# Performance work log

Hardware: AMD Instinct MI355X
Metric: run time of the kernel (lower is better)

The kernel has to match this reference:

```python
import jax, jax.numpy as jnp
import numpy as np

CONV = 49
LAYERS = 4
EDGE_DIM = 10
MSG_H = 3
EPS = 1e-5

def setup_inputs() -> dict:
    key = jax.random.key(0)
    ks = jax.random.split(key, 16)
    N, E = 25000, 50000
    x = jax.random.normal(ks[0], (N, 56), dtype=jnp.float32)
    edge_index = jax.random.randint(ks[1], (2, E), 0, N, dtype=jnp.int64)
    edge_attr = jax.random.uniform(ks[2], (E, EDGE_DIM), dtype=jnp.float32)
    s = 0.1
    return {
        'x': x,
        'edge_index': edge_index,
        'edge_attr': edge_attr,
        'lin_w': jax.random.normal(ks[3], (56, CONV), dtype=jnp.float32) * s,
        'lin_b': jnp.zeros((CONV,), jnp.float32),
        'mlp_w1': jax.random.normal(ks[4], (LAYERS, EDGE_DIM, MSG_H), dtype=jnp.float32) * s,
        'mlp_b1': jnp.zeros((LAYERS, MSG_H), jnp.float32),
        'mlp_w2': jax.random.normal(ks[5], (LAYERS, MSG_H, CONV * CONV), dtype=jnp.float32) * s,
        'mlp_b2': jnp.zeros((LAYERS, CONV * CONV), jnp.float32),
        'root_w': jax.random.normal(ks[6], (LAYERS, CONV, CONV), dtype=jnp.float32) * s,
        'conv_b': jnp.zeros((LAYERS, CONV), jnp.float32),
        'bn_gamma': jnp.ones((LAYERS, CONV), jnp.float32),
        'bn_beta': jnp.zeros((LAYERS, CONV), jnp.float32),
    }

def reference(x, edge_index, edge_attr, lin_w, lin_b, mlp_w1, mlp_b1, mlp_w2, mlp_b2, root_w, conv_b, bn_gamma, bn_beta):
    N = x.shape[0]
    E = edge_attr.shape[0]
    src, dst = edge_index[0], edge_index[1]
    # input atom projection
    h = jax.nn.leaky_relu(x @ lin_w + lin_b)
    # scatter-mean denominator (count clamped at 1, as in PyG)
    deg = jax.ops.segment_sum(jnp.ones((E,), h.dtype), dst, num_segments=N)
    denom = jnp.maximum(deg, 1.0)[:, None]
    xs = [h]
    for l in range(LAYERS):
        hc = xs[l]
        # edge MLP -> per-edge [CONV, CONV] weight matrix
        ew = jax.nn.relu(edge_attr @ mlp_w1[l] + mlp_b1[l]) @ mlp_w2[l] + mlp_b2[l]
        ew = ew.reshape(E, CONV, CONV)
        # gather src features, per-edge matvec, scatter-mean to dst
        msg = jnp.einsum('ei,eio->eo', hc[src], ew)
        agg = jax.ops.segment_sum(msg, dst, num_segments=N) / denom
        # NNConv root weight + bias
        out = agg + hc @ root_w[l] + conv_b[l]
        # BatchNorm1d (training-mode batch statistics, biased variance)
        mu = out.mean(axis=0)
        var = out.var(axis=0)
        out = (out - mu) * jax.lax.rsqrt(var + EPS) * bn_gamma[l] + bn_beta[l]
        out = jax.nn.leaky_relu(out)
        xs.append(out)
    # JK = 'sum' over layers 0..num_layer-1 (first 4 entries of x_list)
    return xs[0] + xs[1] + xs[2] + xs[3]
```

## Files before the change

kernel.cpp:

```cpp
#include <hip/hip_runtime.h>


#define N 25000
#define E 50000
#define C 49
#define C2 196
#define SLOPE 0.01f
#define BPN 32
#define GK 2
#define NPB 8
#define NREP 8

__device__ __forceinline__ float leaky(float v) { return v > 0.f ? v : SLOPE * v; }
#define RFL(x) __builtin_amdgcn_readfirstlane(x)

__global__ void deg_kernel(const int* __restrict__ ei, int* __restrict__ deg) {
    int e = blockIdx.x * 256 + threadIdx.x;
    if (e < E) atomicAdd(&deg[ei[E + e]], 1);
}

__global__ __launch_bounds__(1024) void scan_kernel(const int* __restrict__ deg,
                                                    int* __restrict__ rowptr) {
    __shared__ int wsum[16];
    int t = threadIdx.x, lane = t & 63, wv = t >> 6;
    int base = t * 25;
    int loc[25];
    int run = 0;
#pragma unroll
    for (int i = 0; i < 25; i++) {
        loc[i] = run;
        int idx = base + i;
        run += (idx < N) ? deg[idx] : 0;
    }
    int inc = run;
#pragma unroll
    for (int s = 1; s < 64; s <<= 1) {
        int v = __shfl_up(inc, s, 64);
        if (lane >= s) inc += v;
    }
    if (lane == 63) wsum[wv] = inc;
    __syncthreads();
    if (t < 16) {
        int v = wsum[t];
#pragma unroll
        for (int s = 1; s < 16; s <<= 1) {
            int u = __shfl_up(v, s, 64);
            if (t >= s) v += u;
        }
        wsum[t] = v;
    }
    __syncthreads();
    int pbase = inc - run + (wv ? wsum[wv - 1] : 0);
#pragma unroll
    for (int i = 0; i < 25; i++) {
        int idx = base + i;
        if (idx <= N) rowptr[idx] = pbase + loc[i];
    }
}

__global__ void scatter_kernel(const int* __restrict__ ei, const float* __restrict__ ea,
                               const float* __restrict__ w1, const float* __restrict__ b1,
                               const int* __restrict__ rowptr, int* __restrict__ cnt,
                               float* __restrict__ PK) {
    int e = blockIdx.x * 256 + threadIdx.x;
    if (e >= E) return;
    int s = ei[e], d = ei[E + e];
    int pos = rowptr[d] + atomicAdd(&cnt[d], 1);
    float a[10];
#pragma unroll
    for (int j = 0; j < 10; j++) a[j] = ea[e * 10 + j];
#pragma unroll
    for (int l = 0; l < 3; l++) {
        float tk[3];
#pragma unroll
        for (int k = 0; k < 3; k++) {
            float acc = b1[l * 3 + k];
#pragma unroll
            for (int j = 0; j < 10; j++) acc += a[j] * w1[l * 30 + j * 3 + k];
            tk[k] = fmaxf(acc, 0.f);
        }
        float4 rec = make_float4(__int_as_float(s), tk[0], tk[1], tk[2]);
        *reinterpret_cast<float4*>(PK + ((size_t)l * E + pos) * 4) = rec;
    }
}

__device__ __forceinline__ void gemm_phase(const float (*hs)[52], int base, int nv,
                                           const float* __restrict__ w2,
                                           const float* __restrict__ b2,
                                           const float* __restrict__ rw,
                                           const float* __restrict__ cb,
                                           float* __restrict__ U, float* __restrict__ Rt,
                                           int t) {
    if (t >= 245) return;
    int k = t / C, o = t % C;
    const float* Wp = (k < 3 ? w2 + k * (C * C) : (k == 3 ? b2 : rw)) + o;
    float bias = (k == 4) ? cb[o] : 0.f;
    float w[52];
#pragma unroll
    for (int i = 0; i < C; i++) w[i] = Wp[i * C];
    w[49] = w[50] = w[51] = 0.f;
#pragma unroll 2
    for (int n = 0; n < nv; n++) {
        float acc = bias;
#pragma unroll
        for (int i4 = 0; i4 < 13; i4++) {
            float4 hv = *reinterpret_cast<const float4*>(&hs[n][i4 * 4]);
            acc += hv.x * w[i4 * 4] + hv.y * w[i4 * 4 + 1] + hv.z * w[i4 * 4 + 2] +
                   hv.w * w[i4 * 4 + 3];
        }
        if (k < 4) U[(size_t)(base + n) * C2 + o * 4 + k] = acc;
        else Rt[(size_t)(base + n) * C + o] = acc;
    }
}

__global__ __launch_bounds__(256) void h2u0_kernel(
    const float* __restrict__ x, const float* __restrict__ lw, const float* __restrict__ lb,
    const float* __restrict__ w2, const float* __restrict__ b2, const float* __restrict__ rw,
    const float* __restrict__ cb, float* __restrict__ out, float* __restrict__ U,
    float* __restrict__ Rt) {
    __shared__ float xs[BPN][56];
    __shared__ float hs[BPN][52];
    int t = threadIdx.x, base = blockIdx.x * BPN;
    int nv = min(BPN, N - base);
    for (int e = t; e < nv * 56; e += 256) xs[e / 56][e % 56] = x[(size_t)base * 56 + e];
    for (int j = t; j < BPN * 3; j += 256) hs[j / 3][C + (j % 3)] = 0.f;
    __syncthreads();
    int r = t >> 6, c = t & 63;
    if (c < C) {
        float w[56];
#pragma unroll
        for (int i = 0; i < 56; i++) w[i] = lw[i * C + c];
        float bias = lb[c];
        for (int n = r; n < nv; n += 4) {
            float acc = bias;
#pragma unroll
            for (int i4 = 0; i4 < 14; i4++) {
                float4 hv = *reinterpret_cast<const float4*>(&xs[n][i4 * 4]);
                acc += hv.x * w[i4 * 4] + hv.y * w[i4 * 4 + 1] + hv.z * w[i4 * 4 + 2] +
                       hv.w * w[i4 * 4 + 3];
            }
            acc = leaky(acc);
            out[(size_t)(base + n) * C + c] = acc;
            hs[n][c] = acc;
        }
    }
    __syncthreads();
    gemm_phase(hs, base, nv, w2, b2, rw, cb, U, Rt, t);
}

__global__ __launch_bounds__(256) void uni_kernel(
    const float* __restrict__ in, const float* __restrict__ stRaw,
    const float* __restrict__ gm, const float* __restrict__ bt,
    const float* __restrict__ w2, const float* __restrict__ b2,
    const float* __restrict__ rw, const float* __restrict__ cb,
    float* __restrict__ out, float* __restrict__ U, float* __restrict__ Rt) {
    __shared__ float hs[BPN][52];
    __shared__ float scl[64], sft[64];
    int t = threadIdx.x, base = blockIdx.x * BPN;
    int nv = min(BPN, N - base);
    if (t < C) {
        float S = 0.f, Q = 0.f;
#pragma unroll
        for (int r = 0; r < NREP; r++) {
            S += stRaw[r * 128 + t];
            Q += stRaw[r * 128 + 64 + t];
        }
        float mu = S * (1.0f / N);
        float var = Q * (1.0f / N) - mu * mu;
        float sc = rsqrtf(var + 1e-5f) * gm[t];
        scl[t] = sc;
        sft[t] = bt[t] - mu * sc;
    }
    for (int j = t; j < BPN * 3; j += 256) hs[j / 3][C + j % 3] = 0.f;
    __syncthreads();
    for (int e = t; e < nv * C; e += 256) {
        int n = e / C, i = e % C;
        float v = in[(size_t)base * C + e];
        v = leaky(v * scl[i] + sft[i]);
        out[(size_t)base * C + e] += v;
        hs[n][i] = v;
    }
    __syncthreads();
    gemm_phase(hs, base, nv, w2, b2, rw, cb, U, Rt, t);
}

__global__ __launch_bounds__(256) void gathpre_kernel(
    const int* __restrict__ rowptr, const float* __restrict__ PK, const float* __restrict__ U,
    const float* __restrict__ Rt, float* __restrict__ pre, float* __restrict__ st) {
    __shared__ float red[8][64];
    int t = threadIdx.x, wv = t >> 6, c = t & 63;
    int n0 = blockIdx.x * NPB + wv * GK;
    float s = 0.f, q = 0.f;
    int nend = min(n0 + GK, N);
    const float4* PK4 = reinterpret_cast<const float4*>(PK);
    for (int n = n0; n < nend; n++) {
        int nu = RFL(n);
        int j0 = RFL(rowptr[nu]);
        int j1 = RFL(rowptr[nu + 1]);
        if (c < C) {
            float rr = Rt[(size_t)nu * C + c];
            float a0 = 0.f, a1 = 0.f, a2 = 0.f, a3 = 0.f;
            int jc = max(j1 - 1, j0);
            int j = j0;
            do {
#define EDGE_TERM(K, AK)                                                          \
                {                                                                 \
                    int jj = min(j + K, jc);                                      \
                    float4 m = PK4[jj];                                           \
                    int sidx = RFL(__float_as_int(m.x));                          \
                    sidx = min(max(sidx, 0), N - 1);                              \
                    float4 u = *reinterpret_cast<const float4*>(                  \
                        U + (size_t)sidx * C2 + c * 4);                           \
                    float sc = (j + K < j1) ? 1.f : 0.f;                          \
                    AK += sc * (m.y * u.x + m.z * u.y + m.w * u.z + u.w);         \
                }
                EDGE_TERM(0, a0)
                EDGE_TERM(1, a1)
                EDGE_TERM(2, a2)
                EDGE_TERM(3, a3)
#undef EDGE_TERM
                j += 4;
            } while (j < j1);
            float inv = 1.0f / fmaxf((float)(j1 - j0), 1.0f);
            float acc = (a0 + a1 + a2 + a3) * inv + rr;
            pre[(size_t)nu * C + c] = acc;
            s += acc;
            q += acc * acc;
        }
    }
    red[wv][c] = s;
    red[4 + wv][c] = q;
    __syncthreads();
    if (t < C) {
        float* slot = st + (blockIdx.x & (NREP - 1)) * 128;
        float S = red[0][t] + red[1][t] + red[2][t] + red[3][t];
        float Q = red[4][t] + red[5][t] + red[6][t] + red[7][t];
        atomicAdd(&slot[t], S);
        atomicAdd(&slot[64 + t], Q);
    }
}

__global__ __launch_bounds__(256) void fnorm_kernel(const float* __restrict__ pre,
                                                    const float* __restrict__ stRaw,
                                                    const float* __restrict__ gm,
                                                    const float* __restrict__ bt,
                                                    float* __restrict__ out) {
    __shared__ float scl[64], sft[64];
    int t = threadIdx.x;
    if (t < C) {
        float S = 0.f, Q = 0.f;
#pragma unroll
        for (int r = 0; r < NREP; r++) {
            S += stRaw[r * 128 + t];
            Q += stRaw[r * 128 + 64 + t];
        }
        float mu = S * (1.0f / N);
        float var = Q * (1.0f / N) - mu * mu;
        float sc = rsqrtf(var + 1e-5f) * gm[t];
        scl[t] = sc;
        sft[t] = bt[t] - mu * sc;
    }
    __syncthreads();
    for (int idx = blockIdx.x * 256 + t; idx < N * C; idx += gridDim.x * 256) {
        int c = idx % C;
        out[idx] += leaky(pre[idx] * scl[c] + sft[c]);
    }
}

extern "C" void kernel_launch(void* const* d_in, const int* in_sizes, int n_in,
                              void* d_out, int out_size, void* d_ws, size_t ws_size,
                              hipStream_t stream) {
    const float* x  = (const float*)d_in[0];
    const int* ei   = (const int*)d_in[1];
    const float* ea = (const float*)d_in[2];
    const float* lw = (const float*)d_in[3];
    const float* lb = (const float*)d_in[4];
    const float* w1 = (const float*)d_in[5];
    const float* b1 = (const float*)d_in[6];
    const float* w2 = (const float*)d_in[7];
    const float* b2 = (const float*)d_in[8];
    const float* rw = (const float*)d_in[9];
    const float* cb = (const float*)d_in[10];
    const float* gm = (const float*)d_in[11];
    const float* bt = (const float*)d_in[12];
    float* out = (float*)d_out;

    float* ws     = (float*)d_ws;
    int*   deg    = (int*)ws;
    int*   cnt    = deg + N;
    float* st     = (float*)(cnt + N);
    int*   rowptr = (int*)(st + 3 * 1024);
    float* PK     = (float*)(rowptr + N + 1);
    float* agg    = PK + (size_t)12 * E;
    float* Rt     = agg + (size_t)N * C;
    float* U      = Rt + (size_t)N * C;

    hipMemsetAsync(deg, 0, (size_t)(2 * N + 3 * 1024) * sizeof(int), stream);
    deg_kernel<<<(E + 255) / 256, 256, 0, stream>>>(ei, deg);
    scan_kernel<<<1, 1024, 0, stream>>>(deg, rowptr);
    scatter_kernel<<<(E + 255) / 256, 256, 0, stream>>>(ei, ea, w1, b1, rowptr, cnt, PK);
    h2u0_kernel<<<(N + BPN - 1) / BPN, 256, 0, stream>>>(x, lw, lb, w2, b2, rw, cb, out, U, Rt);

    const int GPB = (N + NPB - 1) / NPB;
    for (int l = 0; l < 3; l++) {
        if (l > 0) {
            uni_kernel<<<(N + BPN - 1) / BPN, 256, 0, stream>>>(
                agg, st + (size_t)(l - 1) * 1024, gm + (l - 1) * C, bt + (l - 1) * C,
                w2 + (size_t)l * 3 * C * C, b2 + (size_t)l * C * C,
                rw + (size_t)l * C * C, cb + l * C, out, U, Rt);
        }
        gathpre_kernel<<<GPB, 256, 0, stream>>>(
            rowptr, PK + (size_t)l * E * 4, U, Rt, agg, st + (size_t)l * 1024);
    }
    fnorm_kernel<<<512, 256, 0, stream>>>(agg, st + 2 * 1024, gm + 2 * C, bt + 2 * C, out);
}
```

Measured before the change: 240.2 us.

## Fuse degree count, scan and memset into one kernel; merge scatter with input projection

Replaces the memset, degree-atomic kernel and scan kernel with a single one-block kernel that counts degrees in shared memory in two halves, scans them, and initializes rowptr, cnt and the stats buffer. The edge scatter kernel and the input projection kernel are merged into one launch split by block index, with cnt pre-seeded to rowptr so the scatter needs only one atomic. This cuts launches and small serial kernels, but the single-block degree pass reads all edges twice from one CU, which may be slower than the parallel atomic version.

```diff
diff --git a/kernel.cpp b/kernel.cpp
--- a/kernel.cpp
+++ b/kernel.cpp
@@ -10,78 +10,74 @@
 #define GK 2
 #define NPB 8
 #define NREP 8
+#define HALF 12500
 
 __device__ __forceinline__ float leaky(float v) { return v > 0.f ? v : SLOPE * v; }
 #define RFL(x) __builtin_amdgcn_readfirstlane(x)
 
-__global__ void deg_kernel(const int* __restrict__ ei, int* __restrict__ deg) {
-    int e = blockIdx.x * 256 + threadIdx.x;
-    if (e < E) atomicAdd(&deg[ei[E + e]], 1);
-}
-
-__global__ __launch_bounds__(1024) void scan_kernel(const int* __restrict__ deg,
-                                                    int* __restrict__ rowptr) {
+__global__ __launch_bounds__(1024) void degscan_kernel(const int* __restrict__ ei,
+                                                       int* __restrict__ rowptr,
+                                                       int* __restrict__ cnt,
+                                                       float* __restrict__ st) {
+    __shared__ int sdeg[HALF + 44];
     __shared__ int wsum[16];
+    __shared__ int carrys;
     int t = threadIdx.x, lane = t & 63, wv = t >> 6;
-    int base = t * 25;
-    int loc[25];
-    int run = 0;
-#pragma unroll
-    for (int i = 0; i < 25; i++) {
-        loc[i] = run;
-        int idx = base + i;
-        run += (idx < N) ? deg[idx] : 0;
-    }
-    int inc = run;
-#pragma unroll
-    for (int s = 1; s < 64; s <<= 1) {
-        int v = __shfl_up(inc, s, 64);
-        if (lane >= s) inc += v;
-    }
-    if (lane == 63) wsum[wv] = inc;
-    __syncthreads();
-    if (t < 16) {
-        int v = wsum[t];
-#pragma unroll
-        for (int s = 1; s < 16; s <<= 1) {
-            int u = __shfl_up(v, s, 64);
-            if (t >= s) v += u;
-        }
-        wsum[t] = v;
-    }
-    __syncthreads();
-    int pbase = inc - run + (wv ? wsum[wv - 1] : 0);
-#pragma unroll
-    for (int i = 0; i < 25; i++) {
-        int idx = base + i;
-        if (idx <= N) rowptr[idx] = pbase + loc[i];
-    }
-}
-
-__global__ void scatter_kernel(const int* __restrict__ ei, const float* __restrict__ ea,
-                               const float* __restrict__ w1, const float* __restrict__ b1,
-                               const int* __restrict__ rowptr, int* __restrict__ cnt,
-                               float* __restrict__ PK) {
-    int e = blockIdx.x * 256 + threadIdx.x;
-    if (e >= E) return;
-    int s = ei[e], d = ei[E + e];
-    int pos = rowptr[d] + atomicAdd(&cnt[d], 1);
-    float a[10];
-#pragma unroll
-    for (int j = 0; j < 10; j++) a[j] = ea[e * 10 + j];
-#pragma unroll
-    for (int l = 0; l < 3; l++) {
-        float tk[3];
-#pragma unroll
-        for (int k = 0; k < 3; k++) {
-            float acc = b1[l * 3 + k];
-#pragma unroll
-            for (int j = 0; j < 10; j++) acc += a[j] * w1[l * 30 + j * 3 + k];
-            tk[k] = fmaxf(acc, 0.f);
-        }
-        float4 rec = make_float4(__int_as_float(s), tk[0], tk[1], tk[2]);
-        *reinterpret_cast<float4*>(PK + ((size_t)l * E + pos) * 4) = rec;
-    }
+    if (t == 0) carrys = 0;
+    for (int i = t; i < 3 * 1024; i += 1024) st[i] = 0.f;
+#pragma unroll 1
+    for (int half = 0; half < 2; half++) {
+        int lo = half * HALF;
+        for (int i = t; i < HALF; i += 1024) sdeg[i] = 0;
+        __syncthreads();
+        for (int e = t; e < E; e += 1024) {
+            int d = ei[E + e] - lo;
+            if ((unsigned)d < (unsigned)HALF) atomicAdd(&sdeg[d], 1);
+        }
+        __syncthreads();
+        int base = t * 13;
+        int loc[13];
+        int run = 0;
+#pragma unroll
+        for (int i = 0; i < 13; i++) {
+            loc[i] = run;
+            int idx = base + i;
+            run += (idx < HALF) ? sdeg[idx] : 0;
+        }
+        int inc = run;
+#pragma unroll
+        for (int s = 1; s < 64; s <<= 1) {
+            int v = __shfl_up(inc, s, 64);
+            if (lane >= s) inc += v;
+        }
+        if (lane == 63) wsum[wv] = inc;
+        __syncthreads();
+        if (t < 16) {
+            int v = wsum[t];
+#pragma unroll
+            for (int s = 1; s < 16; s <<= 1) {
+                int u = __shfl_up(v, s, 64);
+                if (t >= s) v += u;
+            }
+            wsum[t] = v;
+        }
+        __syncthreads();
+        int pbase = carrys + inc - run + (wv ? wsum[wv - 1] : 0);
+#pragma unroll
+        for (int i = 0; i < 13; i++) {
+            int idx = base + i;
+            int g = lo + idx;
+            if (idx < HALF && g < N) {
+                int v = pbase + loc[i];
+                rowptr[g] = v;
+                cnt[g] = v;
+            }
+        }
+        __syncthreads();
+        if (t == 0) carrys += wsum[15];
+        __syncthreads();
+    }
+    if (t == 0) rowptr[N] = E;
 }
 
 __device__ __forceinline__ void gemm_phase(const float (*hs)[52], int base, int nv,
@@ -113,39 +109,65 @@
     }
 }
 
-__global__ __launch_bounds__(256) void h2u0_kernel(
+__global__ __launch_bounds__(256) void fuse2_kernel(
     const float* __restrict__ x, const float* __restrict__ lw, const float* __restrict__ lb,
     const float* __restrict__ w2, const float* __restrict__ b2, const float* __restrict__ rw,
-    const float* __restrict__ cb, float* __restrict__ out, float* __restrict__ U,
-    float* __restrict__ Rt) {
+    const float* __restrict__ cb, const int* __restrict__ ei, const float* __restrict__ ea,
+    const float* __restrict__ w1, const float* __restrict__ b1, int* __restrict__ cnt,
+    float* __restrict__ PK, float* __restrict__ out, float* __restrict__ U,
+    float* __restrict__ Rt, int HB) {
     __shared__ float xs[BPN][56];
     __shared__ float hs[BPN][52];
-    int t = threadIdx.x, base = blockIdx.x * BPN;
-    int nv = min(BPN, N - base);
-    for (int e = t; e < nv * 56; e += 256) xs[e / 56][e % 56] = x[(size_t)base * 56 + e];
-    for (int j = t; j < BPN * 3; j += 256) hs[j / 3][C + (j % 3)] = 0.f;
-    __syncthreads();
-    int r = t >> 6, c = t & 63;
-    if (c < C) {
-        float w[56];
-#pragma unroll
-        for (int i = 0; i < 56; i++) w[i] = lw[i * C + c];
-        float bias = lb[c];
-        for (int n = r; n < nv; n += 4) {
-            float acc = bias;
-#pragma unroll
-            for (int i4 = 0; i4 < 14; i4++) {
-                float4 hv = *reinterpret_cast<const float4*>(&xs[n][i4 * 4]);
-                acc += hv.x * w[i4 * 4] + hv.y * w[i4 * 4 + 1] + hv.z * w[i4 * 4 + 2] +
-                       hv.w * w[i4 * 4 + 3];
+    int t = threadIdx.x;
+    if ((int)blockIdx.x < HB) {
+        int base = blockIdx.x * BPN;
+        int nv = min(BPN, N - base);
+        for (int e = t; e < nv * 56; e += 256) xs[e / 56][e % 56] = x[(size_t)base * 56 + e];
+        for (int j = t; j < BPN * 3; j += 256) hs[j / 3][C + (j % 3)] = 0.f;
+        __syncthreads();
+        int r = t >> 6, c = t & 63;
+        if (c < C) {
+            float w[56];
+#pragma unroll
+            for (int i = 0; i < 56; i++) w[i] = lw[i * C + c];
+            float bias = lb[c];
+            for (int n = r; n < nv; n += 4) {
+                float acc = bias;
+#pragma unroll
+                for (int i4 = 0; i4 < 14; i4++) {
+                    float4 hv = *reinterpret_cast<const float4*>(&xs[n][i4 * 4]);
+                    acc += hv.x * w[i4 * 4] + hv.y * w[i4 * 4 + 1] + hv.z * w[i4 * 4 + 2] +
+                           hv.w * w[i4 * 4 + 3];
+                }
+                acc = leaky(acc);
+                out[(size_t)(base + n) * C + c] = acc;
+                hs[n][c] = acc;
             }
-            acc = leaky(acc);
-            out[(size_t)(base + n) * C + c] = acc;
-            hs[n][c] = acc;
-        }
-    }
-    __syncthreads();
-    gemm_phase(hs, base, nv, w2, b2, rw, cb, U, Rt, t);
+        }
+        __syncthreads();
+        gemm_phase(hs, base, nv, w2, b2, rw, cb, U, Rt, t);
+    } else {
+        int e = (blockIdx.x - HB) * 256 + t;
+        if (e >= E) return;
+        int s = ei[e], d = ei[E + e];
+        int pos = atomicAdd(&cnt[d], 1);
+        float a[10];
+#pragma unroll
+        for (int j = 0; j < 10; j++) a[j] = ea[e * 10 + j];
+#pragma unroll
+        for (int l = 0; l < 3; l++) {
+            float tk[3];
+#pragma unroll
+            for (int k = 0; k < 3; k++) {
+                float acc = b1[l * 3 + k];
+#pragma unroll
+                for (int j = 0; j < 10; j++) acc += a[j] * w1[l * 30 + j * 3 + k];
+                tk[k] = fmaxf(acc, 0.f);
+            }
+            float4 rec = make_float4(__int_as_float(s), tk[0], tk[1], tk[2]);
+            *reinterpret_cast<float4*>(PK + ((size_t)l * E + pos) * 4) = rec;
+        }
+    }
 }
 
 __global__ __launch_bounds__(256) void uni_kernel(
@@ -286,25 +308,24 @@
     float* out = (float*)d_out;
 
     float* ws     = (float*)d_ws;
-    int*   deg    = (int*)ws;
-    int*   cnt    = deg + N;
-    float* st     = (float*)(cnt + N);
-    int*   rowptr = (int*)(st + 3 * 1024);
-    float* PK     = (float*)(rowptr + N + 1);
+    int*   cnt    = (int*)ws;
+    int*   rowptr = cnt + N;
+    float* st     = (float*)(rowptr + N + 1);
+    float* PK     = st + 3 * 1024;
     float* agg    = PK + (size_t)12 * E;
     float* Rt     = agg + (size_t)N * C;
     float* U      = Rt + (size_t)N * C;
 
-    hipMemsetAsync(deg, 0, (size_t)(2 * N + 3 * 1024) * sizeof(int), stream);
-    deg_kernel<<<(E + 255) / 256, 256, 0, stream>>>(ei, deg);
-    scan_kernel<<<1, 1024, 0, stream>>>(deg, rowptr);
-    scatter_kernel<<<(E + 255) / 256, 256, 0, stream>>>(ei, ea, w1, b1, rowptr, cnt, PK);
-    h2u0_kernel<<<(N + BPN - 1) / BPN, 256, 0, stream>>>(x, lw, lb, w2, b2, rw, cb, out, U, Rt);
-
+    const int HB = (N + BPN - 1) / BPN;
+    const int SB = (E + 255) / 256;
     const int GPB = (N + NPB - 1) / NPB;
+
+    degscan_kernel<<<1, 1024, 0, stream>>>(ei, rowptr, cnt, st);
+    fuse2_kernel<<<HB + SB, 256, 0, stream>>>(x, lw, lb, w2, b2, rw, cb, ei, ea, w1, b1,
+                                              cnt, PK, out, U, Rt, HB);
     for (int l = 0; l < 3; l++) {
         if (l > 0) {
-            uni_kernel<<<(N + BPN - 1) / BPN, 256, 0, stream>>>(
+            uni_kernel<<<HB, 256, 0, stream>>>(
                 agg, st + (size_t)(l - 1) * 1024, gm + (l - 1) * C, bt + (l - 1) * C,
                 w2 + (size_t)l * 3 * C * C, b2 + (size_t)l * C * C,
                 rw + (size_t)l * C * C, cb + l * C, out, U, Rt);
```

Measured after the change: 256.0 us. 6.6% more time.

## Fuse degree count into projection kernel and seed scatter offsets in scan

Applied to the files above, without the earlier changes.

Degree counting now runs as extra blocks inside the input projection/U-precompute kernel, so it no longer needs its own launch. The scan kernel loads degrees into shared memory, zeroes the BN statistics buffer itself, and writes the exclusive prefix into both rowptr and cnt. The scatter then takes its slot with a single atomicAdd on cnt and no rowptr lookup. The memset shrinks to the cnt array only. The aim is fewer launches and less memset work in the preprocessing chain. The cost is that the 100 KB shared array in the single-block scan must fit in the LDS size available to one block.

```diff
diff --git a/kernel.cpp b/kernel.cpp
--- a/kernel.cpp
+++ b/kernel.cpp
@@ -13,76 +13,6 @@
 
 __device__ __forceinline__ float leaky(float v) { return v > 0.f ? v : SLOPE * v; }
 #define RFL(x) __builtin_amdgcn_readfirstlane(x)
-
-__global__ void deg_kernel(const int* __restrict__ ei, int* __restrict__ deg) {
-    int e = blockIdx.x * 256 + threadIdx.x;
-    if (e < E) atomicAdd(&deg[ei[E + e]], 1);
-}
-
-__global__ __launch_bounds__(1024) void scan_kernel(const int* __restrict__ deg,
-                                                    int* __restrict__ rowptr) {
-    __shared__ int wsum[16];
-    int t = threadIdx.x, lane = t & 63, wv = t >> 6;
-    int base = t * 25;
-    int loc[25];
-    int run = 0;
-#pragma unroll
-    for (int i = 0; i < 25; i++) {
-        loc[i] = run;
-        int idx = base + i;
-        run += (idx < N) ? deg[idx] : 0;
-    }
-    int inc = run;
-#pragma unroll
-    for (int s = 1; s < 64; s <<= 1) {
-        int v = __shfl_up(inc, s, 64);
-        if (lane >= s) inc += v;
-    }
-    if (lane == 63) wsum[wv] = inc;
-    __syncthreads();
-    if (t < 16) {
-        int v = wsum[t];
-#pragma unroll
-        for (int s = 1; s < 16; s <<= 1) {
-            int u = __shfl_up(v, s, 64);
-            if (t >= s) v += u;
-        }
-        wsum[t] = v;
-    }
-    __syncthreads();
-    int pbase = inc - run + (wv ? wsum[wv - 1] : 0);
-#pragma unroll
-    for (int i = 0; i < 25; i++) {
-        int idx = base + i;
-        if (idx <= N) rowptr[idx] = pbase + loc[i];
-    }
-}
-
-__global__ void scatter_kernel(const int* __restrict__ ei, const float* __restrict__ ea,
-                               const float* __restrict__ w1, const float* __restrict__ b1,
-                               const int* __restrict__ rowptr, int* __restrict__ cnt,
-                               float* __restrict__ PK) {
-    int e = blockIdx.x * 256 + threadIdx.x;
-    if (e >= E) return;
-    int s = ei[e], d = ei[E + e];
-    int pos = rowptr[d] + atomicAdd(&cnt[d], 1);
-    float a[10];
-#pragma unroll
-    for (int j = 0; j < 10; j++) a[j] = ea[e * 10 + j];
-#pragma unroll
-    for (int l = 0; l < 3; l++) {
-        float tk[3];
-#pragma unroll
-        for (int k = 0; k < 3; k++) {
-            float acc = b1[l * 3 + k];
-#pragma unroll
-            for (int j = 0; j < 10; j++) acc += a[j] * w1[l * 30 + j * 3 + k];
-            tk[k] = fmaxf(acc, 0.f);
-        }
-        float4 rec = make_float4(__int_as_float(s), tk[0], tk[1], tk[2]);
-        *reinterpret_cast<float4*>(PK + ((size_t)l * E + pos) * 4) = rec;
-    }
-}
 
 __device__ __forceinline__ void gemm_phase(const float (*hs)[52], int base, int nv,
                                            const float* __restrict__ w2,
@@ -113,14 +43,21 @@
     }
 }
 
-__global__ __launch_bounds__(256) void h2u0_kernel(
+__global__ __launch_bounds__(256) void fuseA_kernel(
+    const int* __restrict__ ei, int* __restrict__ cnt,
     const float* __restrict__ x, const float* __restrict__ lw, const float* __restrict__ lb,
     const float* __restrict__ w2, const float* __restrict__ b2, const float* __restrict__ rw,
     const float* __restrict__ cb, float* __restrict__ out, float* __restrict__ U,
-    float* __restrict__ Rt) {
+    float* __restrict__ Rt, int DB) {
     __shared__ float xs[BPN][56];
     __shared__ float hs[BPN][52];
-    int t = threadIdx.x, base = blockIdx.x * BPN;
+    int t = threadIdx.x;
+    if ((int)blockIdx.x < DB) {
+        int e = blockIdx.x * 256 + t;
+        if (e < E) atomicAdd(&cnt[ei[E + e]], 1);
+        return;
+    }
+    int base = (blockIdx.x - DB) * BPN;
     int nv = min(BPN, N - base);
     for (int e = t; e < nv * 56; e += 256) xs[e / 56][e % 56] = x[(size_t)base * 56 + e];
     for (int j = t; j < BPN * 3; j += 256) hs[j / 3][C + (j % 3)] = 0.f;
@@ -146,6 +83,82 @@
     }
     __syncthreads();
     gemm_phase(hs, base, nv, w2, b2, rw, cb, U, Rt, t);
+}
+
+__global__ __launch_bounds__(1024) void scanseed_kernel(int* __restrict__ cnt,
+                                                        int* __restrict__ rowptr,
+                                                        float* __restrict__ st) {
+    __shared__ int sl[N];
+    __shared__ int wsum[16];
+    int t = threadIdx.x, lane = t & 63, wv = t >> 6;
+    for (int i = t; i < 3 * 1024; i += 1024) st[i] = 0.f;
+    for (int i = t; i < N; i += 1024) sl[i] = cnt[i];
+    __syncthreads();
+    int base = t * 25;
+    int loc[25];
+    int run = 0;
+#pragma unroll
+    for (int i = 0; i < 25; i++) {
+        loc[i] = run;
+        int idx = base + i;
+        run += (idx < N) ? sl[idx] : 0;
+    }
+    int inc = run;
+#pragma unroll
+    for (int s = 1; s < 64; s <<= 1) {
+        int v = __shfl_up(inc, s, 64);
+        if (lane >= s) inc += v;
+    }
+    if (lane == 63) wsum[wv] = inc;
+    __syncthreads();
+    if (t < 16) {
+        int v = wsum[t];
+#pragma unroll
+        for (int s = 1; s < 16; s <<= 1) {
+            int u = __shfl_up(v, s, 64);
+            if (t >= s) v += u;
+        }
+        wsum[t] = v;
+    }
+    __syncthreads();
+    int pbase = inc - run + (wv ? wsum[wv - 1] : 0);
+#pragma unroll
+    for (int i = 0; i < 25; i++) {
+        int idx = base + i;
+        if (idx < N) sl[idx] = pbase + loc[i];
+    }
+    __syncthreads();
+    for (int i = t; i < N; i += 1024) {
+        int v = sl[i];
+        rowptr[i] = v;
+        cnt[i] = v;
+    }
+    if (t == 0) rowptr[N] = E;
+}
+
+__global__ void scatter_kernel(const int* __restrict__ ei, const float* __restrict__ ea,
+                               const float* __restrict__ w1, const float* __restrict__ b1,
+                               int* __restrict__ cnt, float* __restrict__ PK) {
+    int e = blockIdx.x * 256 + threadIdx.x;
+    if (e >= E) return;
+    int s = ei[e], d = ei[E + e];
+    int pos = atomicAdd(&cnt[d], 1);
+    float a[10];
+#pragma unroll
+    for (int j = 0; j < 10; j++) a[j] = ea[e * 10 + j];
+#pragma unroll
+    for (int l = 0; l < 3; l++) {
+        float tk[3];
+#pragma unroll
+        for (int k = 0; k < 3; k++) {
+            float acc = b1[l * 3 + k];
+#pragma unroll
+            for (int j = 0; j < 10; j++) acc += a[j] * w1[l * 30 + j * 3 + k];
+            tk[k] = fmaxf(acc, 0.f);
+        }
+        float4 rec = make_float4(__int_as_float(s), tk[0], tk[1], tk[2]);
+        *reinterpret_cast<float4*>(PK + ((size_t)l * E + pos) * 4) = rec;
+    }
 }
 
 __global__ __launch_bounds__(256) void uni_kernel(
@@ -286,25 +299,26 @@
     float* out = (float*)d_out;
 
     float* ws     = (float*)d_ws;
-    int*   deg    = (int*)ws;
-    int*   cnt    = deg + N;
-    float* st     = (float*)(cnt + N);
-    int*   rowptr = (int*)(st + 3 * 1024);
-    float* PK     = (float*)(rowptr + N + 1);
+    int*   cnt    = (int*)ws;
+    int*   rowptr = cnt + N;
+    float* st     = (float*)(rowptr + N + 1);
+    float* PK     = st + 3 * 1024;
     float* agg    = PK + (size_t)12 * E;
     float* Rt     = agg + (size_t)N * C;
     float* U      = Rt + (size_t)N * C;
 
-    hipMemsetAsync(deg, 0, (size_t)(2 * N + 3 * 1024) * sizeof(int), stream);
-    deg_kernel<<<(E + 255) / 256, 256, 0, stream>>>(ei, deg);
-    scan_kernel<<<1, 1024, 0, stream>>>(deg, rowptr);
-    scatter_kernel<<<(E + 255) / 256, 256, 0, stream>>>(ei, ea, w1, b1, rowptr, cnt, PK);
-    h2u0_kernel<<<(N + BPN - 1) / BPN, 256, 0, stream>>>(x, lw, lb, w2, b2, rw, cb, out, U, Rt);
-
+    const int DB = (E + 255) / 256;
+    const int HB = (N + BPN - 1) / BPN;
     const int GPB = (N + NPB - 1) / NPB;
+
+    hipMemsetAsync(cnt, 0, (size_t)N * sizeof(int), stream);
+    fuseA_kernel<<<DB + HB, 256, 0, stream>>>(ei, cnt, x, lw, lb, w2, b2, rw, cb,
+                                              out, U, Rt, DB);
+    scanseed_kernel<<<1, 1024, 0, stream>>>(cnt, rowptr, st);
+    scatter_kernel<<<DB, 256, 0, stream>>>(ei, ea, w1, b1, cnt, PK);
     for (int l = 0; l < 3; l++) {
         if (l > 0) {
-            uni_kernel<<<(N + BPN - 1) / BPN, 256, 0, stream>>>(
+            uni_kernel<<<HB, 256, 0, stream>>>(
                 agg, st + (size_t)(l - 1) * 1024, gm + (l - 1) * C, bt + (l - 1) * C,
                 w2 + (size_t)l * 3 * C * C, b2 + (size_t)l * C * C,
                 rw + (size_t)l * C * C, cb + l * C, out, U, Rt);
```

Result: faster. 228.5 us (-4.9%).
